# Optimization experiments

Hardware: AMD Instinct MI355X
Metric: run time of the kernel (lower is better)

The kernel has to match this reference:

```python
import jax, jax.numpy as jnp
import numpy as np

B, T, D, H, C = 8, 512, 1024, 16, 10   # batch, seq (T_out+1), d=nb_lon*nb_lat, heads, classes
L = 4                                   # effective layers = n - 1 (ModuleLists hold n-1 entries)
DH = D // H
RD = float(np.sqrt(D))
EPS = 1e-5


def make_pos():
    # pos[t, 2k] = sin((t+1)*w_k), pos[t, 2k+1] = sin((t+1)*w_k + pi/2)
    t = np.arange(1, T + 1, dtype=np.float32)[:, None]          # [T,1]
    kk = np.arange(D // 2, dtype=np.float32)
    omega = np.repeat(1.0 / 1000.0 ** (2.0 * kk / D), 2)[None]  # [1,D]
    phase = np.tile(np.array([0.0, np.pi / 2], dtype=np.float32), D // 2)[None]
    return jnp.asarray(np.sin(t * omega + phase), dtype=jnp.float32)


def setup_inputs() -> dict:
    key = jax.random.key(0)
    ks = jax.random.split(key, 12)
    s = 0.02
    inp = {
        'x': jax.random.normal(ks[0], (B, T, D), jnp.float32),
        'k': jax.random.normal(ks[1], (B, H, T, DH), jnp.float32),
        'v': jax.random.normal(ks[2], (B, H, T, DH), jnp.float32),
        'pos': make_pos(),
        'Wq1': jax.random.normal(ks[3], (L, D, D), jnp.float32) * s,
        'Wk1': jax.random.normal(ks[4], (L, D, D), jnp.float32) * s,
        'Wv1': jax.random.normal(ks[5], (L, D, D), jnp.float32) * s,
        'Wq2': jax.random.normal(ks[6], (L, D, D), jnp.float32) * s,
        'Wfc': jax.random.normal(ks[7], (L, D, D), jnp.float32) * s,
        'bfc': jnp.zeros((L, D), jnp.float32),
        'g1': jnp.ones((L - 1, D), jnp.float32),
        'b1': jnp.zeros((L - 1, D), jnp.float32),
        'g2': jnp.ones((L, D), jnp.float32),
        'b2': jnp.zeros((L, D), jnp.float32),
        'g3': jnp.ones((L, D), jnp.float32),
        'b3': jnp.zeros((L, D), jnp.float32),
        # xavier_uniform on [1, C-1]
        'cutoff': jax.random.uniform(ks[8], (1, C - 1), jnp.float32,
                                     -np.sqrt(6.0 / C), np.sqrt(6.0 / C)),
    }
    return inp


def _ln(x, g, b):
    m = jnp.mean(x, axis=-1, keepdims=True)
    var = jnp.var(x, axis=-1, keepdims=True)
    return (x - m) / jnp.sqrt(var + EPS) * g + b


def _self_attn(x, Wq, Wk, Wv):
    # nn.Linear: y = x @ W.T ; no causal mask (masking defaults to False)
    q = (x @ Wq.T).reshape(B, T, H, DH)
    kk = (x @ Wk.T).reshape(B, T, H, DH)
    vv = (x @ Wv.T).reshape(B, T, H, DH)
    a = jnp.einsum('bqhe,bkhe->bhqk', q, kk) / RD
    a = jax.nn.softmax(a, axis=-1)
    o = jnp.einsum('bhqk,bkhe->bqhe', a, vv).reshape(B, T, D)
    return x + o


def _cross_attn(x, Wq, k, v, mask):
    q = (x @ Wq.T).reshape(B, T, H, DH)
    a = jnp.einsum('bqhe,bhke->bhqk', q, k) / RD
    a = jnp.where(mask, -jnp.inf, a)  # causal mask on cross scores (intended semantics)
    a = jax.nn.softmax(a, axis=-1)
    o = jnp.einsum('bhqk,bhke->bqhe', a, v).reshape(B, T, D)
    return x + o


def reference(x, k, v, pos, Wq1, Wk1, Wv1, Wq2, Wfc, bfc,
              g1, b1, g2, b2, g3, b3, cutoff):
    x = x + pos
    mask = jnp.triu(jnp.ones((T, T), bool), 1)
    for i in range(L):
        if i != 0:
            x = _ln(x, g1[i - 1], b1[i - 1])
        x = _self_attn(x, Wq1[i], Wk1[i], Wv1[i])
        x = _ln(x, g2[i], b2[i])
        x = _cross_attn(x, Wq2[i], k, v, mask)
        x = _ln(x, g3[i], b3[i])
        x = jax.nn.relu(x @ Wfc[i].T + bfc[i]) + x
    # ordinal sigmoid head: cumulative cutoffs, adjacent sigmoid differences
    b = jnp.cumsum(jnp.concatenate([cutoff[:, :1], cutoff[:, 1:] ** 2], axis=1), axis=1)  # [1,C-1]
    sig = jax.nn.sigmoid(b[0] - x[..., None])  # [B,T,D,C-1]
    probs = jnp.concatenate(
        [sig[..., :1], sig[..., 1:] - sig[..., :-1], 1.0 - sig[..., -1:]], axis=-1)
    return probs
```

## Files before the change

kernel.cpp:

```cpp
#include <hip/hip_runtime.h>


#define BB   8
#define TT   512
#define DD   1024
#define HH   16
#define DHH  64
#define LLAY 4
#define MM   (BB*TT)
#define MD   ((size_t)MM*DD)
#define INV_RD (1.0f/32.0f)
#define LNEPS 1e-5f

typedef unsigned short ushort_t;
typedef __attribute__((ext_vector_type(8))) short short8;
typedef __attribute__((ext_vector_type(4))) float floatx4;

__device__ inline ushort_t f2bf(float f) {
  unsigned u = __builtin_bit_cast(unsigned, f);
  unsigned r = (u + 0x7FFFu + ((u >> 16) & 1u)) >> 16;
  return (ushort_t)r;
}

__device__ inline size_t bhtd(int m, int cg) {
  return ((size_t)((m >> 9) * HH + (cg >> 6)) * TT + (m & (TT - 1))) * DHH + (cg & 63);
}

__global__ __launch_bounds__(256) void cast_all_k(
    const float* __restrict__ Wq1, const float* __restrict__ Wk1,
    const float* __restrict__ Wv1, const float* __restrict__ Wq2f,
    const float* __restrict__ Wfcf, const float* __restrict__ kin,
    const float* __restrict__ vin, const float* __restrict__ x,
    const float* __restrict__ pos,
    ushort_t* __restrict__ wqkv, ushort_t* __restrict__ wq2,
    ushort_t* __restrict__ wfc, ushort_t* __restrict__ kinbf,
    ushort_t* __restrict__ vinbf, float* __restrict__ cur,
    ushort_t* __restrict__ act_bf) {
  int seg = blockIdx.x >> 12;
  size_t j = ((size_t)(blockIdx.x & 4095)) * 256 + threadIdx.x;
  if (seg == 7) {
    int dq  = (int)(j & 255);
    int row = (int)(j >> 8);
    int t   = row & (TT - 1);
    float4 a = ((const float4*)x)[j];
    float4 p = ((const float4*)pos)[(size_t)t * 256 + dq];
    a.x += p.x; a.y += p.y; a.z += p.z; a.w += p.w;
    ((float4*)cur)[j] = a;
    ushort4 b; b.x = f2bf(a.x); b.y = f2bf(a.y); b.z = f2bf(a.z); b.w = f2bf(a.w);
    ((ushort4*)act_bf)[j] = b;
    return;
  }
  const float* src;
  switch (seg) {
    case 0: src = Wq1; break;
    case 1: src = Wk1; break;
    case 2: src = Wv1; break;
    case 3: src = Wq2f; break;
    case 4: src = Wfcf; break;
    case 5: src = kin; break;
    default: src = vin; break;
  }
  float4 v = ((const float4*)src)[j];
  ushort4 o; o.x = f2bf(v.x); o.y = f2bf(v.y); o.z = f2bf(v.z); o.w = f2bf(v.w);
  if (seg < 3) {
    int d4 = (int)(j & 255);
    int n  = (int)((j >> 8) & 1023);
    int i  = (int)(j >> 18);
    size_t drow = (size_t)i * 3072 + (size_t)seg * 1024 + n;
    ((ushort4*)wqkv)[drow * 256 + d4] = o;
  } else {
    ushort_t* dst = (seg == 3) ? wq2 : (seg == 4) ? wfc : (seg == 5) ? kinbf : vinbf;
    ((ushort4*)dst)[j] = o;
  }
}

__global__ __launch_bounds__(256) void ln_k(const float* __restrict__ in,
                                            float* __restrict__ out,
                                            ushort_t* __restrict__ out_bf,
                                            const float* __restrict__ g,
                                            const float* __restrict__ bt) {
  int row = blockIdx.x;
  int t = threadIdx.x;
  const float4* r4 = (const float4*)(in + (size_t)row * DD);
  float4 v = r4[t];
  float s  = v.x + v.y + v.z + v.w;
  float ss = v.x*v.x + v.y*v.y + v.z*v.z + v.w*v.w;
#pragma unroll
  for (int off = 32; off > 0; off >>= 1) {
    s  += __shfl_down(s, off);
    ss += __shfl_down(ss, off);
  }
  __shared__ float red[8];
  int w = t >> 6;
  if ((t & 63) == 0) { red[w] = s; red[4 + w] = ss; }
  __syncthreads();
  s  = red[0] + red[1] + red[2] + red[3];
  ss = red[4] + red[5] + red[6] + red[7];
  float mean = s * (1.0f / DD);
  float var  = ss * (1.0f / DD) - mean * mean;
  float inv  = rsqrtf(var + LNEPS);
  float4 gv = ((const float4*)g)[t];
  float4 bv = ((const float4*)bt)[t];
  float4 o;
  o.x = (v.x - mean) * inv * gv.x + bv.x;
  o.y = (v.y - mean) * inv * gv.y + bv.y;
  o.z = (v.z - mean) * inv * gv.z + bv.z;
  o.w = (v.w - mean) * inv * gv.w + bv.w;
  ((float4*)(out + (size_t)row * DD))[t] = o;
  ushort4 ob; ob.x = f2bf(o.x); ob.y = f2bf(o.y); ob.z = f2bf(o.z); ob.w = f2bf(o.w);
  ((ushort4*)(out_bf + (size_t)row * DD))[t] = ob;
}

__global__ __launch_bounds__(256) void gemm_mfma_bt_k(const ushort_t* __restrict__ A,
                                                      const ushort_t* __restrict__ W,
                                                      ushort_t* __restrict__ Cout,
                                                      int nbx) {
  __shared__ ushort_t As[128 * 64];
  __shared__ ushort_t Bs[128 * 64];
  int t = threadIdx.x;
  int d = blockIdx.x;
  int chunk = gridDim.x >> 3;
  int logical = (d & 7) * chunk + (d >> 3);
  int bx = logical % nbx, by = logical / nbx;
  int n0 = bx * 128, m0 = by * 128;
  int lane = t & 63, w = t >> 6;
  int wm = (w >> 1) * 64, wn = (w & 1) * 64;
  int fr = lane & 15, q = lane >> 4;
  int arow[4], brow[4];
#pragma unroll
  for (int i = 0; i < 4; i++) { arow[i] = wm + i * 16 + fr; brow[i] = wn + i * 16 + fr; }
  auto* As3 = (__attribute__((address_space(3))) ushort_t*)As;
  auto* Bs3 = (__attribute__((address_space(3))) ushort_t*)Bs;
  floatx4 acc[4][4] = {};
  for (int k0 = 0; k0 < DD; k0 += 64) {
    __syncthreads();
#pragma unroll
    for (int j = 0; j < 4; j++) {
      int e = t + j * 256;
      int row = e >> 3, slot = e & 7;
      int c = slot ^ (row & 7);
      const ushort_t* asrc = A + (size_t)(m0 + row) * DD + k0 + c * 8;
      const ushort_t* wsrc = W + (size_t)(n0 + row) * DD + k0 + c * 8;
      __builtin_amdgcn_global_load_lds(
          (const __attribute__((address_space(1))) unsigned*)asrc,
          (__attribute__((address_space(3))) unsigned*)(As3 + e * 8), 16, 0, 0);
      __builtin_amdgcn_global_load_lds(
          (const __attribute__((address_space(1))) unsigned*)wsrc,
          (__attribute__((address_space(3))) unsigned*)(Bs3 + e * 8), 16, 0, 0);
    }
    __syncthreads();
#pragma unroll
    for (int kk = 0; kk < 2; kk++) {
      short8 af[4], bf[4];
#pragma unroll
      for (int i = 0; i < 4; i++) {
        int ra = arow[i], rb = brow[i];
        af[i] = *(const short8*)(As + ra * 64 + (((kk * 4 + q) ^ (ra & 7)) * 8));
        bf[i] = *(const short8*)(Bs + rb * 64 + (((kk * 4 + q) ^ (rb & 7)) * 8));
      }
#pragma unroll
      for (int i = 0; i < 4; i++)
#pragma unroll
        for (int j = 0; j < 4; j++)
          acc[i][j] = __builtin_amdgcn_mfma_f32_16x16x32_bf16(af[i], bf[j], acc[i][j], 0, 0, 0);
    }
  }
  int orow = m0 + wm + q * 4;
  int ocol = n0 + wn + fr;
  int seg = n0 >> 10;
  ushort_t* Cb = Cout + (size_t)seg * MD;
#pragma unroll
  for (int i = 0; i < 4; i++)
#pragma unroll
    for (int j = 0; j < 4; j++) {
      int cg = (ocol + j * 16) & 1023;
#pragma unroll
      for (int rr = 0; rr < 4; rr++)
        Cb[bhtd(orow + i * 16 + rr, cg)] = f2bf(acc[i][j][rr]);
    }
}

__global__ __launch_bounds__(256) void gemm64_k(const ushort_t* __restrict__ A,
                                                const ushort_t* __restrict__ W,
                                                void* __restrict__ Cout,
                                                const float* __restrict__ bias,
                                                const float* __restrict__ lnres,
                                                const float* __restrict__ cutv,
                                                int mode) {
  __shared__ ushort_t As[128 * 64];
  __shared__ ushort_t Bs[64 * 64];
  int t = threadIdx.x;
  int d = blockIdx.x;
  int logical = (d & 7) * 64 + (d >> 3);
  int bx = logical & 15, by = logical >> 4;
  int n0 = bx * 64, m0 = by * 128;
  int lane = t & 63, w = t >> 6;
  int wm = (w >> 1) * 64, wn = (w & 1) * 32;
  int fr = lane & 15, q = lane >> 4;
  int arow[4], brow[2];
#pragma unroll
  for (int i = 0; i < 4; i++) arow[i] = wm + i * 16 + fr;
#pragma unroll
  for (int j = 0; j < 2; j++) brow[j] = wn + j * 16 + fr;
  auto* As3 = (__attribute__((address_space(3))) ushort_t*)As;
  auto* Bs3 = (__attribute__((address_space(3))) ushort_t*)Bs;
  floatx4 acc[4][2] = {};
  for (int k0 = 0; k0 < DD; k0 += 64) {
    __syncthreads();
#pragma unroll
    for (int j = 0; j < 4; j++) {
      int e = t + j * 256;
      int row = e >> 3, slot = e & 7;
      int c = slot ^ (row & 7);
      const ushort_t* asrc = A + (size_t)(m0 + row) * DD + k0 + c * 8;
      __builtin_amdgcn_global_load_lds(
          (const __attribute__((address_space(1))) unsigned*)asrc,
          (__attribute__((address_space(3))) unsigned*)(As3 + e * 8), 16, 0, 0);
    }
#pragma unroll
    for (int j = 0; j < 2; j++) {
      int e = t + j * 256;
      int row = e >> 3, slot = e & 7;
      int c = slot ^ (row & 7);
      const ushort_t* wsrc = W + (size_t)(n0 + row) * DD + k0 + c * 8;
      __builtin_amdgcn_global_load_lds(
          (const __attribute__((address_space(1))) unsigned*)wsrc,
          (__attribute__((address_space(3))) unsigned*)(Bs3 + e * 8), 16, 0, 0);
    }
    __syncthreads();
#pragma unroll
    for (int kk = 0; kk < 2; kk++) {
      short8 af[4], bf[2];
#pragma unroll
      for (int i = 0; i < 4; i++) {
        int ra = arow[i];
        af[i] = *(const short8*)(As + ra * 64 + (((kk * 4 + q) ^ (ra & 7)) * 8));
      }
#pragma unroll
      for (int j = 0; j < 2; j++) {
        int rb = brow[j];
        bf[j] = *(const short8*)(Bs + rb * 64 + (((kk * 4 + q) ^ (rb & 7)) * 8));
      }
#pragma unroll
      for (int i = 0; i < 4; i++)
#pragma unroll
        for (int j = 0; j < 2; j++)
          acc[i][j] = __builtin_amdgcn_mfma_f32_16x16x32_bf16(af[i], bf[j], acc[i][j], 0, 0, 0);
    }
  }
  int orow = m0 + wm + q * 4;
  if (mode == 1) {
    ushort_t* Cb = (ushort_t*)Cout;
#pragma unroll
    for (int i = 0; i < 4; i++)
#pragma unroll
      for (int j = 0; j < 2; j++) {
        int colg = n0 + wn + j * 16 + fr;
#pragma unroll
        for (int rr = 0; rr < 4; rr++)
          Cb[bhtd(orow + i * 16 + rr, colg)] = f2bf(acc[i][j][rr]);
      }
  } else if (mode == 2) {
    float* C = (float*)Cout;
#pragma unroll
    for (int j = 0; j < 2; j++) {
      int colg = n0 + wn + j * 16 + fr;
      float bv = bias[colg];
#pragma unroll
      for (int i = 0; i < 4; i++)
#pragma unroll
        for (int rr = 0; rr < 4; rr++) {
          size_t idx = (size_t)(orow + i * 16 + rr) * DD + colg;
          C[idx] = fmaxf(acc[i][j][rr] + bv, 0.f) + lnres[idx];
        }
    }
  } else {
    float* H = (float*)Cout;
    float bcum[9];
    bcum[0] = cutv[0];
#pragma unroll
    for (int j = 1; j < 9; j++) { float c = cutv[j]; bcum[j] = bcum[j - 1] + c * c; }
#pragma unroll
    for (int j = 0; j < 2; j++) {
      int colg = n0 + wn + j * 16 + fr;
      float bv = bias[colg];
#pragma unroll
      for (int i = 0; i < 4; i++)
#pragma unroll
        for (int rr = 0; rr < 4; rr++) {
          size_t idx = (size_t)(orow + i * 16 + rr) * DD + colg;
          float xv = fmaxf(acc[i][j][rr] + bv, 0.f) + lnres[idx];
          float ov[10];
          float sp = 1.0f / (1.0f + __expf(xv - bcum[0]));
          ov[0] = sp;
#pragma unroll
          for (int c = 1; c < 9; c++) {
            float sc = 1.0f / (1.0f + __expf(xv - bcum[c]));
            ov[c] = sc - sp;
            sp = sc;
          }
          ov[9] = 1.0f - sp;
          float2* op = (float2*)(H + idx * 10);
#pragma unroll
          for (int c = 0; c < 5; c++) { float2 p; p.x = ov[2 * c]; p.y = ov[2 * c + 1]; op[c] = p; }
        }
    }
  }
}

__global__ __launch_bounds__(256) void attn_mfma_k(const ushort_t* __restrict__ Qb,
                                                   const ushort_t* __restrict__ Kb,
                                                   const ushort_t* __restrict__ Vb,
                                                   const float* __restrict__ resid,
                                                   float* __restrict__ out,
                                                   int cross) {
  __shared__ ushort_t Ks[128 * 64];
  __shared__ ushort_t Vts[64 * 128];
  __shared__ ushort_t QP[64 * 64];
  int t = threadIdx.x, lane = t & 63, w = t >> 6;
  int fr = lane & 15, q8 = lane >> 4;
  int dsp = blockIdx.x;
  int logical = (dsp & 7) * 128 + (dsp >> 3);
  int qt = logical & 7, bh = logical >> 3;
  int b = bh >> 4, h = bh & 15;
  size_t kvbase = (size_t)bh * TT * DHH;
  size_t qbase  = kvbase + (size_t)qt * 64 * DHH;

  auto* QP3 = (__attribute__((address_space(3))) ushort_t*)QP;
  auto* Ks3 = (__attribute__((address_space(3))) ushort_t*)Ks;

#pragma unroll
  for (int j = 0; j < 2; j++) {
    int e = t + j * 256;
    int row = e >> 3, slot = e & 7;
    int c = slot ^ (row & 7);
    const ushort_t* src = Qb + qbase + (size_t)row * 64 + c * 8;
    __builtin_amdgcn_global_load_lds(
        (const __attribute__((address_space(1))) unsigned*)src,
        (__attribute__((address_space(3))) unsigned*)(QP3 + e * 8), 16, 0, 0);
  }
  __syncthreads();

  short8 qf[2];
#pragma unroll
  for (int ks = 0; ks < 2; ks++) {
    int row = w * 16 + fr;
    int slot = (ks * 4 + q8) ^ (row & 7);
    qf[ks] = *(const short8*)(QP + row * 64 + slot * 8);
  }

  float m_i[4], l_i[4];
  floatx4 o_acc[4] = {};
#pragma unroll
  for (int r = 0; r < 4; r++) { m_i[r] = -1e30f; l_i[r] = 0.f; }

  int nch = cross ? ((qt * 64 + 64 + 127) >> 7) : (TT / 128);
  for (int ch = 0; ch < nch; ch++) {
    __syncthreads();
#pragma unroll
    for (int j = 0; j < 4; j++) {
      int e = t + j * 256;
      int row = e >> 3, slot = e & 7;
      int c = slot ^ (row & 7);
      const ushort_t* src = Kb + kvbase + (size_t)(ch * 128 + row) * 64 + c * 8;
      __builtin_amdgcn_global_load_lds(
          (const __attribute__((address_space(1))) unsigned*)src,
          (__attribute__((address_space(3))) unsigned*)(Ks3 + e * 8), 16, 0, 0);
    }
    {
      int kp = t & 31, dhg = (t >> 5) * 8;
      const ushort_t* v0 = Vb + kvbase + (size_t)(ch * 128 + 4 * kp) * 64 + dhg;
      short8 a0 = *(const short8*)v0;
      short8 a1 = *(const short8*)(v0 + 64);
      short8 a2 = *(const short8*)(v0 + 128);
      short8 a3 = *(const short8*)(v0 + 192);
#pragma unroll
      for (int j = 0; j < 8; j++) {
        int dh = dhg + j;
        int slot = (kp >> 1) ^ (dh & 15);
        unsigned p01 = (unsigned)(unsigned short)a0[j] |
                       ((unsigned)(unsigned short)a1[j] << 16);
        unsigned p23 = (unsigned)(unsigned short)a2[j] |
                       ((unsigned)(unsigned short)a3[j] << 16);
        uint2 pk; pk.x = p01; pk.y = p23;
        *(uint2*)(Vts + dh * 128 + slot * 8 + (kp & 1) * 4) = pk;
      }
    }
    __syncthreads();

    floatx4 s[8] = {};
    __builtin_amdgcn_s_setprio(1);
#pragma unroll
    for (int nt = 0; nt < 8; nt++) {
      int key = nt * 16 + fr;
#pragma unroll
      for (int ks = 0; ks < 2; ks++) {
        int slot = (ks * 4 + q8) ^ (key & 7);
        short8 kf = *(const short8*)(Ks + key * 64 + slot * 8);
        s[nt] = __builtin_amdgcn_mfma_f32_16x16x32_bf16(qf[ks], kf, s[nt], 0, 0, 0);
      }
    }
    __builtin_amdgcn_s_setprio(0);
    float sv[8][4];
#pragma unroll
    for (int nt = 0; nt < 8; nt++)
#pragma unroll
      for (int r = 0; r < 4; r++)
        sv[nt][r] = s[nt][r] * INV_RD;
    if (cross && ch == nch - 1) {
#pragma unroll
      for (int nt = 0; nt < 8; nt++) {
        int key_g = ch * 128 + nt * 16 + fr;
#pragma unroll
        for (int r = 0; r < 4; r++) {
          int q_g = qt * 64 + w * 16 + q8 * 4 + r;
          if (key_g > q_g) sv[nt][r] = -1e30f;
        }
      }
    }

#pragma unroll
    for (int r = 0; r < 4; r++) {
      float mch = fmaxf(fmaxf(fmaxf(sv[0][r], sv[1][r]), fmaxf(sv[2][r], sv[3][r])),
                        fmaxf(fmaxf(sv[4][r], sv[5][r]), fmaxf(sv[6][r], sv[7][r])));
#pragma unroll
      for (int off = 1; off < 16; off <<= 1) mch = fmaxf(mch, __shfl_xor(mch, off));
      float mn = fmaxf(m_i[r], mch);
      float alpha = __expf(m_i[r] - mn);
      m_i[r] = mn;
      float rs = 0.f;
#pragma unroll
      for (int nt = 0; nt < 8; nt++) {
        float pe = __expf(sv[nt][r] - mn);
        sv[nt][r] = pe; rs += pe;
      }
#pragma unroll
      for (int off = 1; off < 16; off <<= 1) rs += __shfl_xor(rs, off);
      l_i[r] = l_i[r] * alpha + rs;
#pragma unroll
      for (int nt = 0; nt < 4; nt++) o_acc[nt][r] *= alpha;
    }

    ushort_t* Pw = QP + w * 1024;
#pragma unroll
    for (int hf = 0; hf < 2; hf++) {
#pragma unroll
      for (int n4 = 0; n4 < 4; n4++) {
        int col = n4 * 16 + fr;
#pragma unroll
        for (int r = 0; r < 4; r++) {
          int row = q8 * 4 + r;
          int slot = (col >> 3) ^ (row & 7);
          Pw[row * 64 + slot * 8 + (col & 7)] = f2bf(sv[hf * 4 + n4][r]);
        }
      }
      short8 pf[2];
#pragma unroll
      for (int ks = 0; ks < 2; ks++) {
        int slot = (ks * 4 + q8) ^ (fr & 7);
        pf[ks] = *(const short8*)(Pw + fr * 64 + slot * 8);
      }
      __builtin_amdgcn_s_setprio(1);
#pragma unroll
      for (int dnt = 0; dnt < 4; dnt++) {
        int dh = dnt * 16 + fr;
#pragma unroll
        for (int ks = 0; ks < 2; ks++) {
          int vslot = (hf * 8 + ks * 4 + q8) ^ (dh & 15);
          short8 vf = *(const short8*)(Vts + dh * 128 + vslot * 8);
          o_acc[dnt] = __builtin_amdgcn_mfma_f32_16x16x32_bf16(pf[ks], vf, o_acc[dnt], 0, 0, 0);
        }
      }
      __builtin_amdgcn_s_setprio(0);
    }
  }

  float invl[4];
#pragma unroll
  for (int r = 0; r < 4; r++) invl[r] = 1.0f / l_i[r];
#pragma unroll
  for (int nt = 0; nt < 4; nt++) {
#pragma unroll
    for (int r = 0; r < 4; r++) {
      size_t row_g = (size_t)(b * TT + qt * 64 + w * 16 + q8 * 4 + r);
      size_t idx = row_g * DD + h * DHH + nt * 16 + fr;
      out[idx] = resid[idx] + o_acc[nt][r] * invl[r];
    }
  }
}

extern "C" void kernel_launch(void* const* d_in, const int* in_sizes, int n_in,
                              void* d_out, int out_size, void* d_ws, size_t ws_size,
                              hipStream_t stream) {
  (void)in_sizes; (void)n_in; (void)out_size; (void)ws_size;
  const float* x    = (const float*)d_in[0];
  const float* kin  = (const float*)d_in[1];
  const float* vin  = (const float*)d_in[2];
  const float* pos  = (const float*)d_in[3];
  const float* Wq1  = (const float*)d_in[4];
  const float* Wk1  = (const float*)d_in[5];
  const float* Wv1  = (const float*)d_in[6];
  const float* Wq2  = (const float*)d_in[7];
  const float* Wfc  = (const float*)d_in[8];
  const float* bfc  = (const float*)d_in[9];
  const float* g1   = (const float*)d_in[10];
  const float* b1   = (const float*)d_in[11];
  const float* g2   = (const float*)d_in[12];
  const float* b2   = (const float*)d_in[13];
  const float* g3   = (const float*)d_in[14];
  const float* b3   = (const float*)d_in[15];
  const float* cut  = (const float*)d_in[16];
  float* out = (float*)d_out;

  float* cur = (float*)d_ws;
  float* tmp = cur + MD;
  ushort_t* act_bf = (ushort_t*)(tmp + MD);
  ushort_t* qbf    = act_bf + MD;
  ushort_t* kbf    = qbf + MD;
  ushort_t* vbf    = kbf + MD;
  ushort_t* kinbf  = vbf + MD;
  ushort_t* vinbf  = kinbf + MD;
  ushort_t* wqkv   = vinbf + MD;
  ushort_t* wq2    = wqkv + (size_t)LLAY * 3 * DD * DD;
  ushort_t* wfc    = wq2  + (size_t)LLAY * DD * DD;

  dim3 b256(256);

  cast_all_k<<<8 * 4096, b256, 0, stream>>>(Wq1, Wk1, Wv1, Wq2, Wfc, kin, vin,
                                            x, pos, wqkv, wq2, wfc, kinbf, vinbf,
                                            cur, act_bf);

  for (int i = 0; i < LLAY; i++) {
    const float* attn_in;
    if (i) {
      ln_k<<<MM, b256, 0, stream>>>(cur, tmp, act_bf,
                                    g1 + (size_t)(i - 1) * DD, b1 + (size_t)(i - 1) * DD);
      attn_in = tmp;
    } else {
      attn_in = cur;
    }
    gemm_mfma_bt_k<<<768, b256, 0, stream>>>(act_bf, wqkv + (size_t)i * 3 * DD * DD,
                                             qbf, 24);
    attn_mfma_k<<<1024, b256, 0, stream>>>(qbf, kbf, vbf, attn_in, cur, 0);

    ln_k<<<MM, b256, 0, stream>>>(cur, tmp, act_bf,
                                  g2 + (size_t)i * DD, b2 + (size_t)i * DD);
    gemm64_k<<<512, b256, 0, stream>>>(act_bf, wq2 + (size_t)i * DD * DD,
                                       qbf, nullptr, nullptr, nullptr, 1);
    attn_mfma_k<<<1024, b256, 0, stream>>>(qbf, kinbf, vinbf, tmp, cur, 1);

    ln_k<<<MM, b256, 0, stream>>>(cur, tmp, act_bf,
                                  g3 + (size_t)i * DD, b3 + (size_t)i * DD);
    if (i < LLAY - 1) {
      gemm64_k<<<512, b256, 0, stream>>>(act_bf, wfc + (size_t)i * DD * DD,
                                         cur, bfc + (size_t)i * DD, tmp, nullptr, 2);
    } else {
      gemm64_k<<<512, b256, 0, stream>>>(act_bf, wfc + (size_t)i * DD * DD,
                                         out, bfc + (size_t)i * DD, tmp, cut, 3);
    }
  }
}
```

Measured before the change: 942.8 us.

## Double-buffer K/V tiles in attention and skip unnecessary softmax rescales

The attention kernel now keeps two shared-memory buffers for K and transposed V. The next chunk's K loads (async global-to-LDS) and V transposes are issued while the current chunk is being computed, and V registers are prefetched two chunks ahead, which removes one barrier per iteration. The online softmax also rescales the output accumulators and running sum only when some row's chunk max exceeds its running max by more than 8; otherwise it keeps the old max, which still bounds exponentials to a safe range. In exchange, LDS use roughly doubles (about 72KB per block), which may cut the number of resident blocks per CU.

```diff
diff --git a/kernel.cpp b/kernel.cpp
--- a/kernel.cpp
+++ b/kernel.cpp
@@ -314,8 +314,8 @@
                                                    const float* __restrict__ resid,
                                                    float* __restrict__ out,
                                                    int cross) {
-  __shared__ ushort_t Ks[128 * 64];
-  __shared__ ushort_t Vts[64 * 128];
+  __shared__ ushort_t Ks[2][128 * 64];
+  __shared__ ushort_t Vts[2][64 * 128];
   __shared__ ushort_t QP[64 * 64];
   int t = threadIdx.x, lane = t & 63, w = t >> 6;
   int fr = lane & 15, q8 = lane >> 4;
@@ -327,7 +327,10 @@
   size_t qbase  = kvbase + (size_t)qt * 64 * DHH;
 
   auto* QP3 = (__attribute__((address_space(3))) ushort_t*)QP;
-  auto* Ks3 = (__attribute__((address_space(3))) ushort_t*)Ks;
+  auto* Ks3 = (__attribute__((address_space(3))) ushort_t*)(&Ks[0][0]);
+
+  int nch = cross ? ((qt * 64 + 64 + 127) >> 7) : (TT / 128);
+  int kp = t & 31, dhg = (t >> 5) * 8;
 
 #pragma unroll
   for (int j = 0; j < 2; j++) {
@@ -339,6 +342,24 @@
         (const __attribute__((address_space(1))) unsigned*)src,
         (__attribute__((address_space(3))) unsigned*)(QP3 + e * 8), 16, 0, 0);
   }
+#pragma unroll
+  for (int j = 0; j < 4; j++) {
+    int e = t + j * 256;
+    int row = e >> 3, slot = e & 7;
+    int c = slot ^ (row & 7);
+    const ushort_t* src = Kb + kvbase + (size_t)row * 64 + c * 8;
+    __builtin_amdgcn_global_load_lds(
+        (const __attribute__((address_space(1))) unsigned*)src,
+        (__attribute__((address_space(3))) unsigned*)(Ks3 + e * 8), 16, 0, 0);
+  }
+  short8 va0, va1, va2, va3;
+  {
+    const ushort_t* v0 = Vb + kvbase + (size_t)(4 * kp) * 64 + dhg;
+    va0 = *(const short8*)v0;
+    va1 = *(const short8*)(v0 + 64);
+    va2 = *(const short8*)(v0 + 128);
+    va3 = *(const short8*)(v0 + 192);
+  }
   __syncthreads();
 
   short8 qf[2];
@@ -349,45 +370,68 @@
     qf[ks] = *(const short8*)(QP + row * 64 + slot * 8);
   }
 
+#pragma unroll
+  for (int j = 0; j < 8; j++) {
+    int dh = dhg + j;
+    int slot = (kp >> 1) ^ (dh & 15);
+    unsigned p01 = (unsigned)(unsigned short)va0[j] |
+                   ((unsigned)(unsigned short)va1[j] << 16);
+    unsigned p23 = (unsigned)(unsigned short)va2[j] |
+                   ((unsigned)(unsigned short)va3[j] << 16);
+    uint2 pk; pk.x = p01; pk.y = p23;
+    *(uint2*)(&Vts[0][0] + dh * 128 + slot * 8 + (kp & 1) * 4) = pk;
+  }
+  if (nch > 1) {
+    const ushort_t* v0 = Vb + kvbase + (size_t)(128 + 4 * kp) * 64 + dhg;
+    va0 = *(const short8*)v0;
+    va1 = *(const short8*)(v0 + 64);
+    va2 = *(const short8*)(v0 + 128);
+    va3 = *(const short8*)(v0 + 192);
+  }
+
   float m_i[4], l_i[4];
   floatx4 o_acc[4] = {};
 #pragma unroll
   for (int r = 0; r < 4; r++) { m_i[r] = -1e30f; l_i[r] = 0.f; }
 
-  int nch = cross ? ((qt * 64 + 64 + 127) >> 7) : (TT / 128);
+  int cb = 0;
   for (int ch = 0; ch < nch; ch++) {
     __syncthreads();
-#pragma unroll
-    for (int j = 0; j < 4; j++) {
-      int e = t + j * 256;
-      int row = e >> 3, slot = e & 7;
-      int c = slot ^ (row & 7);
-      const ushort_t* src = Kb + kvbase + (size_t)(ch * 128 + row) * 64 + c * 8;
-      __builtin_amdgcn_global_load_lds(
-          (const __attribute__((address_space(1))) unsigned*)src,
-          (__attribute__((address_space(3))) unsigned*)(Ks3 + e * 8), 16, 0, 0);
-    }
-    {
-      int kp = t & 31, dhg = (t >> 5) * 8;
-      const ushort_t* v0 = Vb + kvbase + (size_t)(ch * 128 + 4 * kp) * 64 + dhg;
-      short8 a0 = *(const short8*)v0;
-      short8 a1 = *(const short8*)(v0 + 64);
-      short8 a2 = *(const short8*)(v0 + 128);
-      short8 a3 = *(const short8*)(v0 + 192);
+
+    if (ch + 1 < nch) {
+#pragma unroll
+      for (int j = 0; j < 4; j++) {
+        int e = t + j * 256;
+        int row = e >> 3, slot = e & 7;
+        int c = slot ^ (row & 7);
+        const ushort_t* src = Kb + kvbase + (size_t)((ch + 1) * 128 + row) * 64 + c * 8;
+        __builtin_amdgcn_global_load_lds(
+            (const __attribute__((address_space(1))) unsigned*)src,
+            (__attribute__((address_space(3))) unsigned*)(Ks3 + (cb ^ 1) * 8192 + e * 8),
+            16, 0, 0);
+      }
+      ushort_t* vdst = &Vts[cb ^ 1][0];
 #pragma unroll
       for (int j = 0; j < 8; j++) {
         int dh = dhg + j;
         int slot = (kp >> 1) ^ (dh & 15);
-        unsigned p01 = (unsigned)(unsigned short)a0[j] |
-                       ((unsigned)(unsigned short)a1[j] << 16);
-        unsigned p23 = (unsigned)(unsigned short)a2[j] |
-                       ((unsigned)(unsigned short)a3[j] << 16);
+        unsigned p01 = (unsigned)(unsigned short)va0[j] |
+                       ((unsigned)(unsigned short)va1[j] << 16);
+        unsigned p23 = (unsigned)(unsigned short)va2[j] |
+                       ((unsigned)(unsigned short)va3[j] << 16);
         uint2 pk; pk.x = p01; pk.y = p23;
-        *(uint2*)(Vts + dh * 128 + slot * 8 + (kp & 1) * 4) = pk;
-      }
-    }
-    __syncthreads();
-
+        *(uint2*)(vdst + dh * 128 + slot * 8 + (kp & 1) * 4) = pk;
+      }
+    }
+    if (ch + 2 < nch) {
+      const ushort_t* v0 = Vb + kvbase + (size_t)((ch + 2) * 128 + 4 * kp) * 64 + dhg;
+      va0 = *(const short8*)v0;
+      va1 = *(const short8*)(v0 + 64);
+      va2 = *(const short8*)(v0 + 128);
+      va3 = *(const short8*)(v0 + 192);
+    }
+
+    const ushort_t* Kcur = &Ks[cb][0];
     floatx4 s[8] = {};
     __builtin_amdgcn_s_setprio(1);
 #pragma unroll
@@ -396,7 +440,7 @@
 #pragma unroll
       for (int ks = 0; ks < 2; ks++) {
         int slot = (ks * 4 + q8) ^ (key & 7);
-        short8 kf = *(const short8*)(Ks + key * 64 + slot * 8);
+        short8 kf = *(const short8*)(Kcur + key * 64 + slot * 8);
         s[nt] = __builtin_amdgcn_mfma_f32_16x16x32_bf16(qf[ks], kf, s[nt], 0, 0, 0);
       }
     }
@@ -419,29 +463,43 @@
       }
     }
 
+    float mch[4];
 #pragma unroll
     for (int r = 0; r < 4; r++) {
-      float mch = fmaxf(fmaxf(fmaxf(sv[0][r], sv[1][r]), fmaxf(sv[2][r], sv[3][r])),
-                        fmaxf(fmaxf(sv[4][r], sv[5][r]), fmaxf(sv[6][r], sv[7][r])));
-#pragma unroll
-      for (int off = 1; off < 16; off <<= 1) mch = fmaxf(mch, __shfl_xor(mch, off));
-      float mn = fmaxf(m_i[r], mch);
-      float alpha = __expf(m_i[r] - mn);
-      m_i[r] = mn;
+      float m8 = fmaxf(fmaxf(fmaxf(sv[0][r], sv[1][r]), fmaxf(sv[2][r], sv[3][r])),
+                       fmaxf(fmaxf(sv[4][r], sv[5][r]), fmaxf(sv[6][r], sv[7][r])));
+#pragma unroll
+      for (int off = 1; off < 16; off <<= 1) m8 = fmaxf(m8, __shfl_xor(m8, off));
+      mch[r] = m8;
+    }
+    bool need = (mch[0] > m_i[0] + 8.f) || (mch[1] > m_i[1] + 8.f) ||
+                (mch[2] > m_i[2] + 8.f) || (mch[3] > m_i[3] + 8.f);
+    if (__any(need)) {
+#pragma unroll
+      for (int r = 0; r < 4; r++) {
+        float mn = fmaxf(m_i[r], mch[r]);
+        float alpha = __expf(m_i[r] - mn);
+        m_i[r] = mn;
+        l_i[r] *= alpha;
+#pragma unroll
+        for (int nt = 0; nt < 4; nt++) o_acc[nt][r] *= alpha;
+      }
+    }
+#pragma unroll
+    for (int r = 0; r < 4; r++) {
       float rs = 0.f;
 #pragma unroll
       for (int nt = 0; nt < 8; nt++) {
-        float pe = __expf(sv[nt][r] - mn);
+        float pe = __expf(sv[nt][r] - m_i[r]);
         sv[nt][r] = pe; rs += pe;
       }
 #pragma unroll
       for (int off = 1; off < 16; off <<= 1) rs += __shfl_xor(rs, off);
-      l_i[r] = l_i[r] * alpha + rs;
-#pragma unroll
-      for (int nt = 0; nt < 4; nt++) o_acc[nt][r] *= alpha;
+      l_i[r] += rs;
     }
 
     ushort_t* Pw = QP + w * 1024;
+    const ushort_t* Vcur = &Vts[cb][0];
 #pragma unroll
     for (int hf = 0; hf < 2; hf++) {
 #pragma unroll
@@ -467,12 +525,13 @@
 #pragma unroll
         for (int ks = 0; ks < 2; ks++) {
           int vslot = (hf * 8 + ks * 4 + q8) ^ (dh & 15);
-          short8 vf = *(const short8*)(Vts + dh * 128 + vslot * 8);
+          short8 vf = *(const short8*)(Vcur + dh * 128 + vslot * 8);
           o_acc[dnt] = __builtin_amdgcn_mfma_f32_16x16x32_bf16(pf[ks], vf, o_acc[dnt], 0, 0, 0);
         }
       }
       __builtin_amdgcn_s_setprio(0);
     }
+    cb ^= 1;
   }
 
   float invl[4];
```

Result: no change. 960.2 us (+1.8%).
